# Kernel optimization log

Measured on AMD Instinct MI355X. Metric: run time of the kernel, lower is better.

The kernel has to match this reference:

```python
import jax, jax.numpy as jnp
import numpy as np

B, S, D, F, H, E = 4, 1024, 512, 2048, 8, 8
LN_EPS = 1e-5


def setup_inputs() -> dict:
    key = jax.random.key(0)
    ks = jax.random.split(key, 8)
    sd = 1.0 / np.sqrt(D)
    return {
        'x': jax.random.normal(ks[0], (B, S, D), jnp.float32),
        'in_proj_w': jax.random.normal(ks[1], (3 * D, D), jnp.float32) * sd,
        'in_proj_b': jnp.zeros((3 * D,), jnp.float32),
        'out_proj_w': jax.random.normal(ks[2], (D, D), jnp.float32) * sd,
        'out_proj_b': jnp.zeros((D,), jnp.float32),
        'ln1_g': jnp.ones((D,), jnp.float32),
        'ln1_b': jnp.zeros((D,), jnp.float32),
        'ln2_g': jnp.ones((D,), jnp.float32),
        'ln2_b': jnp.zeros((D,), jnp.float32),
        'router_w': jax.random.normal(ks[3], (D, E), jnp.float32) * sd,
        'wi': jax.random.normal(ks[4], (E, D, F), jnp.float32) * sd,
        'wo': jax.random.normal(ks[5], (E, F, D), jnp.float32) * (1.0 / np.sqrt(F)),
        'expert_capacity': 256,
    }


def _layernorm(x, g, b):
    mu = jnp.mean(x, axis=-1, keepdims=True)
    var = jnp.var(x, axis=-1, keepdims=True)
    return (x - mu) * jax.lax.rsqrt(var + LN_EPS) * g + b


def _mha(x, in_w, in_b, out_w, out_b):
    # torch nn.MultiheadAttention, batch_first, self-attention, no mask
    qkv = x @ in_w.T + in_b                         # [B,S,3D]
    q, k, v = jnp.split(qkv, 3, axis=-1)
    hd = D // H

    def heads(t):
        return t.reshape(B, S, H, hd).transpose(0, 2, 1, 3)  # [B,H,S,hd]

    q, k, v = heads(q), heads(k), heads(v)
    scores = jnp.einsum('bhqd,bhkd->bhqk', q, k) / np.sqrt(hd)
    attn = jax.nn.softmax(scores, axis=-1)
    o = jnp.einsum('bhqk,bhkd->bhqd', attn, v)
    o = o.transpose(0, 2, 1, 3).reshape(B, S, D)
    return o @ out_w.T + out_b


def _router(x, router_w, capacity):
    # Switch-style top-1 router with per-(batch,expert) capacity
    logits = x.astype(jnp.float32) @ router_w       # [B,S,E]
    probs = jax.nn.softmax(logits, axis=-1)
    idx = jnp.argmax(probs, axis=-1)                # [B,S]
    one_hot = jax.nn.one_hot(idx, E, dtype=probs.dtype)
    pos = jnp.cumsum(one_hot, axis=1)               # position within each expert queue
    keep = one_hot * (pos <= capacity).astype(probs.dtype)
    expert_mask = keep * probs                      # dispatch mask scaled by router prob
    return expert_mask, probs, logits


def reference(x, in_proj_w, in_proj_b, out_proj_w, out_proj_b,
              ln1_g, ln1_b, ln2_g, ln2_b, router_w, wi, wo, expert_capacity):
    # self-attention block (post-norm)
    residual = x
    a = _mha(x, in_proj_w, in_proj_b, out_proj_w, out_proj_b)
    h = _layernorm(residual + a, ln1_g, ln1_b)

    # sparse MoE FFN
    expert_mask, _, router_logits = _router(h, router_w, expert_capacity)
    residual = h
    moe = jnp.zeros_like(h)
    for e in range(E):  # fixed small expert loop; masked-dense == gather/FFN/scatter
        y = jax.nn.gelu(h @ wi[e], approximate=False) @ wo[e]
        moe = moe + expert_mask[..., e:e + 1] * y

    out = _layernorm(residual + moe, ln2_g, ln2_b)
    return out, router_logits, expert_mask
```

## Files before the change

### kernel.cpp

```cpp
#include <hip/hip_runtime.h>
#include <math.h>

#define SEQ 1024
#define NTOK 4096
#define DM 512
#define FF 2048
#define NE 8

typedef __attribute__((ext_vector_type(8))) short bf16x8;
typedef __attribute__((ext_vector_type(4))) float f32x4;

__device__ __forceinline__ short f2bf(float f) {
  unsigned u = __float_as_uint(f);
  unsigned r = (u + 0x7FFFu + ((u >> 16) & 1u)) >> 16;
  return (short)r;
}
__device__ __forceinline__ float bf2f(short h) {
  return __uint_as_float(((unsigned)(unsigned short)h) << 16);
}

#define GLOAD_LDS16(g, l) __builtin_amdgcn_global_load_lds( \
    (const __attribute__((address_space(1))) void*)(g),     \
    (__attribute__((address_space(3))) void*)(l), 16, 0, 0)

__global__ __launch_bounds__(256) void split3_kernel(
    const float* __restrict__ x, short* __restrict__ xh, short* __restrict__ xl,
    const float* __restrict__ w1, short* __restrict__ w1h, short* __restrict__ w1l,
    const float* __restrict__ w2, short* __restrict__ w2h, short* __restrict__ w2l) {
  const int bid = blockIdx.x;
  const float* src; short* hi; short* lo; size_t off;
  if (bid < 1024)      { src = x;  hi = xh;  lo = xl;  off = (size_t)bid * 2048; }
  else if (bid < 1408) { src = w1; hi = w1h; lo = w1l; off = (size_t)(bid - 1024) * 2048; }
  else                 { src = w2; hi = w2h; lo = w2l; off = (size_t)(bid - 1408) * 2048; }
  const size_t base = off + threadIdx.x * 8;
  float4 v0 = *reinterpret_cast<const float4*>(src + base);
  float4 v1 = *reinterpret_cast<const float4*>(src + base + 4);
  short h[8]; short l[8];
  float v[8] = {v0.x, v0.y, v0.z, v0.w, v1.x, v1.y, v1.z, v1.w};
#pragma unroll
  for (int i = 0; i < 8; ++i) {
    h[i] = f2bf(v[i]);
    l[i] = f2bf(v[i] - bf2f(h[i]));
  }
  *reinterpret_cast<short4*>(hi + base)     = make_short4(h[0], h[1], h[2], h[3]);
  *reinterpret_cast<short4*>(hi + base + 4) = make_short4(h[4], h[5], h[6], h[7]);
  *reinterpret_cast<short4*>(lo + base)     = make_short4(l[0], l[1], l[2], l[3]);
  *reinterpret_cast<short4*>(lo + base + 4) = make_short4(l[4], l[5], l[6], l[7]);
}

__global__ __launch_bounds__(256) void gemm_split_db(const short* __restrict__ Ah, const short* __restrict__ Al,
    const short* __restrict__ Bh, const short* __restrict__ Bl,
    const float* __restrict__ bias, const float* __restrict__ resid, float* __restrict__ C,
    int N, int K) {
  __shared__ __align__(16) short AsH[2][2048], AsL[2][2048], BsH[2][2048], BsL[2][2048];
  const int n0 = blockIdx.x * 64, m0 = blockIdx.y * 64;
  const int tid = threadIdx.x;
  const int lane = tid & 63, w = tid >> 6;
  const int quad = lane >> 4, l15 = lane & 15;
  const int wm = (w & 1) * 32, wn = (w >> 1) * 32;
  const int sr = tid >> 2, sc = (tid & 3) * 8;
  const short* Ahp = Ah + (size_t)(m0 + sr) * K + sc;
  const short* Alp = Al + (size_t)(m0 + sr) * K + sc;
  const short* Bhp = Bh + (size_t)(n0 + sr) * K + sc;
  const short* Blp = Bl + (size_t)(n0 + sr) * K + sc;
  GLOAD_LDS16(Ahp, &AsH[0][tid * 8]);
  GLOAD_LDS16(Alp, &AsL[0][tid * 8]);
  GLOAD_LDS16(Bhp, &BsH[0][tid * 8]);
  GLOAD_LDS16(Blp, &BsL[0][tid * 8]);
  __syncthreads();
  f32x4 acc[2][2];
#pragma unroll
  for (int i = 0; i < 2; ++i)
#pragma unroll
    for (int j = 0; j < 2; ++j) acc[i][j] = (f32x4){0.f, 0.f, 0.f, 0.f};
  for (int kt = 0; kt < K; kt += 32) {
    const int cur = (kt >> 5) & 1;
    if (kt + 32 < K) {
      const int nxt = cur ^ 1;
      GLOAD_LDS16(Ahp + kt + 32, &AsH[nxt][tid * 8]);
      GLOAD_LDS16(Alp + kt + 32, &AsL[nxt][tid * 8]);
      GLOAD_LDS16(Bhp + kt + 32, &BsH[nxt][tid * 8]);
      GLOAD_LDS16(Blp + kt + 32, &BsL[nxt][tid * 8]);
    }
    bf16x8 ah[2], al[2], bh[2], bl[2];
#pragma unroll
    for (int i = 0; i < 2; ++i) {
      ah[i] = *reinterpret_cast<const bf16x8*>(&AsH[cur][(wm + i * 16 + l15) * 32 + quad * 8]);
      al[i] = *reinterpret_cast<const bf16x8*>(&AsL[cur][(wm + i * 16 + l15) * 32 + quad * 8]);
      bh[i] = *reinterpret_cast<const bf16x8*>(&BsH[cur][(wn + i * 16 + l15) * 32 + quad * 8]);
      bl[i] = *reinterpret_cast<const bf16x8*>(&BsL[cur][(wn + i * 16 + l15) * 32 + quad * 8]);
    }
#pragma unroll
    for (int i = 0; i < 2; ++i)
#pragma unroll
      for (int j = 0; j < 2; ++j) {
        acc[i][j] = __builtin_amdgcn_mfma_f32_16x16x32_bf16(al[i], bh[j], acc[i][j], 0, 0, 0);
        acc[i][j] = __builtin_amdgcn_mfma_f32_16x16x32_bf16(ah[i], bl[j], acc[i][j], 0, 0, 0);
        acc[i][j] = __builtin_amdgcn_mfma_f32_16x16x32_bf16(ah[i], bh[j], acc[i][j], 0, 0, 0);
      }
    __syncthreads();
  }
#pragma unroll
  for (int i = 0; i < 2; ++i) {
#pragma unroll
    for (int reg = 0; reg < 4; ++reg) {
      const int row = m0 + wm + i * 16 + quad * 4 + reg;
#pragma unroll
      for (int j = 0; j < 2; ++j) {
        const int col = n0 + wn + j * 16 + l15;
        float v = acc[i][j][reg] + bias[col] + resid[(size_t)row * N + col];
        C[(size_t)row * N + col] = v;
      }
    }
  }
}

__global__ __launch_bounds__(256) void gemm_split_qkv(const short* __restrict__ Ah, const short* __restrict__ Al,
    const short* __restrict__ Bh, const short* __restrict__ Bl, const float* __restrict__ bias,
    short* __restrict__ qkh, short* __restrict__ qkl, short* __restrict__ vh, short* __restrict__ vl) {
  const int K = DM;
  __shared__ __align__(16) short AsH[2][2048], AsL[2][2048], BsH[2][2048], BsL[2][2048];
  const int n0 = blockIdx.x * 64, m0 = blockIdx.y * 64;
  const int tid = threadIdx.x;
  const int lane = tid & 63, w = tid >> 6;
  const int quad = lane >> 4, l15 = lane & 15;
  const int wm = (w & 1) * 32, wn = (w >> 1) * 32;
  const int sr = tid >> 2, sc = (tid & 3) * 8;
  const short* Ahp = Ah + (size_t)(m0 + sr) * K + sc;
  const short* Alp = Al + (size_t)(m0 + sr) * K + sc;
  const short* Bhp = Bh + (size_t)(n0 + sr) * K + sc;
  const short* Blp = Bl + (size_t)(n0 + sr) * K + sc;
  GLOAD_LDS16(Ahp, &AsH[0][tid * 8]);
  GLOAD_LDS16(Alp, &AsL[0][tid * 8]);
  GLOAD_LDS16(Bhp, &BsH[0][tid * 8]);
  GLOAD_LDS16(Blp, &BsL[0][tid * 8]);
  __syncthreads();
  f32x4 acc[2][2];
#pragma unroll
  for (int i = 0; i < 2; ++i)
#pragma unroll
    for (int j = 0; j < 2; ++j) acc[i][j] = (f32x4){0.f, 0.f, 0.f, 0.f};
  for (int kt = 0; kt < K; kt += 32) {
    const int cur = (kt >> 5) & 1;
    if (kt + 32 < K) {
      const int nxt = cur ^ 1;
      GLOAD_LDS16(Ahp + kt + 32, &AsH[nxt][tid * 8]);
      GLOAD_LDS16(Alp + kt + 32, &AsL[nxt][tid * 8]);
      GLOAD_LDS16(Bhp + kt + 32, &BsH[nxt][tid * 8]);
      GLOAD_LDS16(Blp + kt + 32, &BsL[nxt][tid * 8]);
    }
    bf16x8 ah[2], al[2], bh[2], bl[2];
#pragma unroll
    for (int i = 0; i < 2; ++i) {
      ah[i] = *reinterpret_cast<const bf16x8*>(&AsH[cur][(wm + i * 16 + l15) * 32 + quad * 8]);
      al[i] = *reinterpret_cast<const bf16x8*>(&AsL[cur][(wm + i * 16 + l15) * 32 + quad * 8]);
      bh[i] = *reinterpret_cast<const bf16x8*>(&BsH[cur][(wn + i * 16 + l15) * 32 + quad * 8]);
      bl[i] = *reinterpret_cast<const bf16x8*>(&BsL[cur][(wn + i * 16 + l15) * 32 + quad * 8]);
    }
#pragma unroll
    for (int i = 0; i < 2; ++i)
#pragma unroll
      for (int j = 0; j < 2; ++j) {
        acc[i][j] = __builtin_amdgcn_mfma_f32_16x16x32_bf16(al[i], bh[j], acc[i][j], 0, 0, 0);
        acc[i][j] = __builtin_amdgcn_mfma_f32_16x16x32_bf16(ah[i], bl[j], acc[i][j], 0, 0, 0);
        acc[i][j] = __builtin_amdgcn_mfma_f32_16x16x32_bf16(ah[i], bh[j], acc[i][j], 0, 0, 0);
      }
    __syncthreads();
  }
  if (n0 < 1024) {
#pragma unroll
    for (int i = 0; i < 2; ++i) {
#pragma unroll
      for (int reg = 0; reg < 4; ++reg) {
        const int row = m0 + wm + i * 16 + quad * 4 + reg;
#pragma unroll
        for (int j = 0; j < 2; ++j) {
          const int col = n0 + wn + j * 16 + l15;
          float v = acc[i][j][reg] + bias[col];
          short hv = f2bf(v);
          size_t ad = (size_t)row * 1024 + col;
          qkh[ad] = hv;
          qkl[ad] = f2bf(v - bf2f(hv));
        }
      }
    }
  } else {
#pragma unroll
    for (int i = 0; i < 2; ++i) {
      const int row0 = m0 + wm + i * 16 + quad * 4;
      const int bb = row0 >> 10, s0 = row0 & 1023;
#pragma unroll
      for (int j = 0; j < 2; ++j) {
        const int col = n0 + wn + j * 16 + l15;
        const int c2 = col - 1024;
        const int hhd = c2 >> 6, d = c2 & 63;
        const float bc = bias[col];
        float v0 = acc[i][j][0] + bc, v1 = acc[i][j][1] + bc, v2 = acc[i][j][2] + bc, v3 = acc[i][j][3] + bc;
        short4 hv = make_short4(f2bf(v0), f2bf(v1), f2bf(v2), f2bf(v3));
        short4 lv = make_short4(f2bf(v0 - bf2f(hv.x)), f2bf(v1 - bf2f(hv.y)),
                                f2bf(v2 - bf2f(hv.z)), f2bf(v3 - bf2f(hv.w)));
        size_t ad = ((size_t)(bb * 8 + hhd) * 64 + d) * 1024 + s0;
        *reinterpret_cast<short4*>(vh + ad) = hv;
        *reinterpret_cast<short4*>(vl + ad) = lv;
      }
    }
  }
}

__global__ __launch_bounds__(256) void attn_mfma(const short* __restrict__ qkh, const short* __restrict__ qkl,
    const short* __restrict__ vth, const short* __restrict__ vtl,
    float* __restrict__ opart, float* __restrict__ ml) {
  const int qt = blockIdx.x, hh = blockIdx.y;
  const int b = blockIdx.z >> 1, ks = blockIdx.z & 1;
  __shared__ __align__(16) short Kh[4096], Kl[4096], Vh[4096], Vl[4096];
  const int tid = threadIdx.x;
  const int lane = tid & 63, w = tid >> 6;
  const int quad = lane >> 4, l15 = lane & 15;
  const int tok0 = b * SEQ + qt * 64;
  const int srow = tid >> 2, schunk = (tid & 3) * 8;
  bf16x8 qfh[2], qfl[2];
  {
    const size_t qa = (size_t)(tok0 + w * 16 + l15) * 1024 + hh * 64 + quad * 8;
    qfh[0] = *reinterpret_cast<const bf16x8*>(qkh + qa);
    qfh[1] = *reinterpret_cast<const bf16x8*>(qkh + qa + 32);
    qfl[0] = *reinterpret_cast<const bf16x8*>(qkl + qa);
    qfl[1] = *reinterpret_cast<const bf16x8*>(qkl + qa + 32);
  }
  f32x4 oacc[4];
  float m_run[4], l_run[4];
#pragma unroll
  for (int r = 0; r < 4; ++r) { oacc[r] = (f32x4){0.f, 0.f, 0.f, 0.f}; m_run[r] = -1e30f; l_run[r] = 0.f; }
  const size_t kbase = (size_t)(b * SEQ) * 1024 + 512 + hh * 64;
  const size_t vbase = (size_t)(b * 8 + hh) * 64 * 1024;
  for (int kc = ks * 8; kc < ks * 8 + 8; ++kc) {
    const size_t ka = kbase + (size_t)(kc * 64 + srow) * 1024 + schunk;
    GLOAD_LDS16(qkh + ka,      &Kh[tid * 8]);
    GLOAD_LDS16(qkh + ka + 32, &Kh[2048 + tid * 8]);
    GLOAD_LDS16(qkl + ka,      &Kl[tid * 8]);
    GLOAD_LDS16(qkl + ka + 32, &Kl[2048 + tid * 8]);
    const size_t va = vbase + (size_t)srow * 1024 + kc * 64 + schunk;
    GLOAD_LDS16(vth + va,      &Vh[tid * 8]);
    GLOAD_LDS16(vth + va + 32, &Vh[2048 + tid * 8]);
    GLOAD_LDS16(vtl + va,      &Vl[tid * 8]);
    GLOAD_LDS16(vtl + va + 32, &Vl[2048 + tid * 8]);
    __syncthreads();
    f32x4 s[4];
#pragma unroll
    for (int j = 0; j < 4; ++j) s[j] = (f32x4){0.f, 0.f, 0.f, 0.f};
#pragma unroll
    for (int kk = 0; kk < 2; ++kk)
#pragma unroll
      for (int j = 0; j < 4; ++j) {
        bf16x8 kfh = *reinterpret_cast<const bf16x8*>(&Kh[kk * 2048 + (j * 16 + l15) * 32 + quad * 8]);
        bf16x8 kfl = *reinterpret_cast<const bf16x8*>(&Kl[kk * 2048 + (j * 16 + l15) * 32 + quad * 8]);
        s[j] = __builtin_amdgcn_mfma_f32_16x16x32_bf16(qfl[kk], kfh, s[j], 0, 0, 0);
        s[j] = __builtin_amdgcn_mfma_f32_16x16x32_bf16(qfh[kk], kfl, s[j], 0, 0, 0);
        s[j] = __builtin_amdgcn_mfma_f32_16x16x32_bf16(qfh[kk], kfh, s[j], 0, 0, 0);
      }
    __syncthreads();
    float pv[4][4], alpha[4];
#pragma unroll
    for (int reg = 0; reg < 4; ++reg) {
      float mc = fmaxf(fmaxf(s[0][reg], s[1][reg]), fmaxf(s[2][reg], s[3][reg]));
#pragma unroll
      for (int msk = 1; msk < 16; msk <<= 1) mc = fmaxf(mc, __shfl_xor(mc, msk, 64));
      mc *= 0.125f;
      float mn = fmaxf(m_run[reg], mc);
      alpha[reg] = expf(m_run[reg] - mn);
      m_run[reg] = mn;
      float pl = 0.f;
#pragma unroll
      for (int j = 0; j < 4; ++j) { float pp = expf(s[j][reg] * 0.125f - mn); pv[j][reg] = pp; pl += pp; }
#pragma unroll
      for (int msk = 1; msk < 16; msk <<= 1) pl += __shfl_xor(pl, msk, 64);
      l_run[reg] = l_run[reg] * alpha[reg] + pl;
    }
#pragma unroll
    for (int j = 0; j < 4; ++j) {
      oacc[j][0] *= alpha[0]; oacc[j][1] *= alpha[1]; oacc[j][2] *= alpha[2]; oacc[j][3] *= alpha[3];
    }
#pragma unroll
    for (int j = 0; j < 4; ++j) {
      const int cad = (j >> 1) * 2048 + (j & 1) * 16 + l15;
#pragma unroll
      for (int reg = 0; reg < 4; ++reg) {
        const int ad = cad + (w * 16 + quad * 4 + reg) * 32;
        float p = pv[j][reg];
        short hp = f2bf(p);
        Kh[ad] = hp;
        Kl[ad] = f2bf(p - bf2f(hp));
      }
    }
#pragma unroll
    for (int kk = 0; kk < 2; ++kk) {
      bf16x8 pfh = *reinterpret_cast<const bf16x8*>(&Kh[kk * 2048 + (w * 16 + l15) * 32 + quad * 8]);
      bf16x8 pfl = *reinterpret_cast<const bf16x8*>(&Kl[kk * 2048 + (w * 16 + l15) * 32 + quad * 8]);
#pragma unroll
      for (int j = 0; j < 4; ++j) {
        bf16x8 vfh = *reinterpret_cast<const bf16x8*>(&Vh[kk * 2048 + (j * 16 + l15) * 32 + quad * 8]);
        bf16x8 vfl = *reinterpret_cast<const bf16x8*>(&Vl[kk * 2048 + (j * 16 + l15) * 32 + quad * 8]);
        oacc[j] = __builtin_amdgcn_mfma_f32_16x16x32_bf16(pfl, vfh, oacc[j], 0, 0, 0);
        oacc[j] = __builtin_amdgcn_mfma_f32_16x16x32_bf16(pfh, vfl, oacc[j], 0, 0, 0);
        oacc[j] = __builtin_amdgcn_mfma_f32_16x16x32_bf16(pfh, vfh, oacc[j], 0, 0, 0);
      }
    }
    __syncthreads();
  }
  float* op = opart + (size_t)ks * 2097152;
#pragma unroll
  for (int reg = 0; reg < 4; ++reg) {
    const int rloc = w * 16 + quad * 4 + reg;
#pragma unroll
    for (int j = 0; j < 4; ++j)
      op[(size_t)(tok0 + rloc) * 512 + hh * 64 + j * 16 + l15] = oacc[j][reg];
    if (l15 == 0) {
      size_t mli = (((size_t)ks * 32 + b * 8 + hh) * 1024 + qt * 64 + rloc) * 2;
      ml[mli] = m_run[reg];
      ml[mli + 1] = l_run[reg];
    }
  }
}

__global__ __launch_bounds__(64) void combine_attn(const float* __restrict__ opart, const float* __restrict__ ml,
    short* __restrict__ oh, short* __restrict__ ol) {
  const int t = blockIdx.x;
  const int b = t >> 10, s = t & 1023;
  const int tid = threadIdx.x;
#pragma unroll
  for (int hh = 0; hh < 8; ++hh) {
    size_t mli = (((size_t)(b * 8 + hh)) * 1024 + s) * 2;
    float m0 = ml[mli], l0 = ml[mli + 1];
    float m1 = ml[65536 + mli], l1 = ml[65536 + mli + 1];
    float mm = fmaxf(m0, m1);
    float a0 = expf(m0 - mm), a1 = expf(m1 - mm);
    float inv = 1.f / (l0 * a0 + l1 * a1);
    size_t ad = (size_t)t * 512 + hh * 64 + tid;
    float v = (opart[ad] * a0 + opart[2097152 + ad] * a1) * inv;
    short hv = f2bf(v);
    oh[ad] = hv;
    ol[ad] = f2bf(v - bf2f(hv));
  }
}

__global__ __launch_bounds__(64) void ln_router(const float* __restrict__ r1,
    const float* __restrict__ g, const float* __restrict__ bta, const float* __restrict__ rw,
    float* __restrict__ h, float* __restrict__ rlog, float* __restrict__ probs, int* __restrict__ am) {
  const int t = blockIdx.x, tid = threadIdx.x;
  const size_t base = (size_t)t * DM + tid * 8;
  float4 v0 = *reinterpret_cast<const float4*>(r1 + base);
  float4 v1 = *reinterpret_cast<const float4*>(r1 + base + 4);
  float s = v0.x+v0.y+v0.z+v0.w + v1.x+v1.y+v1.z+v1.w;
  float q = v0.x*v0.x+v0.y*v0.y+v0.z*v0.z+v0.w*v0.w + v1.x*v1.x+v1.y*v1.y+v1.z*v1.z+v1.w*v1.w;
#pragma unroll
  for (int m = 1; m < 64; m <<= 1) { s += __shfl_xor(s, m, 64); q += __shfl_xor(q, m, 64); }
  float mean = s * (1.0f/512.0f);
  float var = q * (1.0f/512.0f) - mean * mean;
  float rs = rsqrtf(var + 1e-5f);
  float4 g0 = *reinterpret_cast<const float4*>(g + tid*8);
  float4 g1 = *reinterpret_cast<const float4*>(g + tid*8 + 4);
  float4 b0 = *reinterpret_cast<const float4*>(bta + tid*8);
  float4 b1 = *reinterpret_cast<const float4*>(bta + tid*8 + 4);
  float hv[8];
  hv[0] = (v0.x-mean)*rs*g0.x+b0.x; hv[1] = (v0.y-mean)*rs*g0.y+b0.y;
  hv[2] = (v0.z-mean)*rs*g0.z+b0.z; hv[3] = (v0.w-mean)*rs*g0.w+b0.w;
  hv[4] = (v1.x-mean)*rs*g1.x+b1.x; hv[5] = (v1.y-mean)*rs*g1.y+b1.y;
  hv[6] = (v1.z-mean)*rs*g1.z+b1.z; hv[7] = (v1.w-mean)*rs*g1.w+b1.w;
  *reinterpret_cast<float4*>(h + base)     = make_float4(hv[0], hv[1], hv[2], hv[3]);
  *reinterpret_cast<float4*>(h + base + 4) = make_float4(hv[4], hv[5], hv[6], hv[7]);
  float lg[8] = {0.f,0.f,0.f,0.f,0.f,0.f,0.f,0.f};
  const float* rwp = rw + tid * 64;
#pragma unroll
  for (int r = 0; r < 8; ++r) {
    float4 w0 = *reinterpret_cast<const float4*>(rwp + r * 8);
    float4 w1 = *reinterpret_cast<const float4*>(rwp + r * 8 + 4);
    float hr = hv[r];
    lg[0] += hr * w0.x; lg[1] += hr * w0.y; lg[2] += hr * w0.z; lg[3] += hr * w0.w;
    lg[4] += hr * w1.x; lg[5] += hr * w1.y; lg[6] += hr * w1.z; lg[7] += hr * w1.w;
  }
#pragma unroll
  for (int m = 1; m < 64; m <<= 1) {
#pragma unroll
    for (int e = 0; e < 8; ++e) lg[e] += __shfl_xor(lg[e], m, 64);
  }
  int best = 0; float bv = lg[0];
#pragma unroll
  for (int e = 1; e < 8; ++e) if (lg[e] > bv) { bv = lg[e]; best = e; }
  float se = 0.f;
#pragma unroll
  for (int e = 0; e < 8; ++e) se += expf(lg[e] - bv);
  float inv = 1.f / se;
  if (tid < 8) {
    rlog[t * 8 + tid] = lg[tid];
    probs[t * 8 + tid] = expf(lg[tid] - bv) * inv;
  }
  if (tid == 0) am[t] = best;
}

__global__ __launch_bounds__(64) void ln2_kernel(const float* __restrict__ x, const float* __restrict__ add,
    const int* __restrict__ pos, const int* __restrict__ capp,
    const float* __restrict__ g, const float* __restrict__ bta, float* __restrict__ y) {
  const int t = blockIdx.x, tid = threadIdx.x;
  const size_t base = (size_t)t * DM + tid * 8;
  float4 v0 = *reinterpret_cast<const float4*>(x + base);
  float4 v1 = *reinterpret_cast<const float4*>(x + base + 4);
  if (pos[t] <= *capp) {
    float4 a0 = *reinterpret_cast<const float4*>(add + base);
    float4 a1 = *reinterpret_cast<const float4*>(add + base + 4);
    v0.x += a0.x; v0.y += a0.y; v0.z += a0.z; v0.w += a0.w;
    v1.x += a1.x; v1.y += a1.y; v1.z += a1.z; v1.w += a1.w;
  }
  float s = v0.x+v0.y+v0.z+v0.w + v1.x+v1.y+v1.z+v1.w;
  float q = v0.x*v0.x+v0.y*v0.y+v0.z*v0.z+v0.w*v0.w + v1.x*v1.x+v1.y*v1.y+v1.z*v1.z+v1.w*v1.w;
#pragma unroll
  for (int m = 1; m < 64; m <<= 1) { s += __shfl_xor(s, m, 64); q += __shfl_xor(q, m, 64); }
  float mean = s * (1.0f/512.0f);
  float var = q * (1.0f/512.0f) - mean * mean;
  float rs = rsqrtf(var + 1e-5f);
  float4 g0 = *reinterpret_cast<const float4*>(g + tid*8);
  float4 g1 = *reinterpret_cast<const float4*>(g + tid*8 + 4);
  float4 b0 = *reinterpret_cast<const float4*>(bta + tid*8);
  float4 b1 = *reinterpret_cast<const float4*>(bta + tid*8 + 4);
  float4 o0 = make_float4((v0.x-mean)*rs*g0.x+b0.x, (v0.y-mean)*rs*g0.y+b0.y,
                          (v0.z-mean)*rs*g0.z+b0.z, (v0.w-mean)*rs*g0.w+b0.w);
  float4 o1 = make_float4((v1.x-mean)*rs*g1.x+b1.x, (v1.y-mean)*rs*g1.y+b1.y,
                          (v1.z-mean)*rs*g1.z+b1.z, (v1.w-mean)*rs*g1.w+b1.w);
  *reinterpret_cast<float4*>(y + base) = o0;
  *reinterpret_cast<float4*>(y + base + 4) = o1;
}

__global__ __launch_bounds__(256) void scan_kernel(const int* __restrict__ am, const float* __restrict__ probs,
    const int* __restrict__ capp, float* __restrict__ emask, int* __restrict__ pos, int* __restrict__ cnt) {
  const int bx = blockIdx.x;
  const int b = bx >> 3, e = bx & 7;
  const int tid = threadIdx.x;
  const int cap = *capp;
  __shared__ int arr[256];
  const int s_base = tid * 4;
  int f[4], incl[4];
  int c = 0;
#pragma unroll
  for (int i = 0; i < 4; ++i) {
    f[i] = (am[b * SEQ + s_base + i] == e) ? 1 : 0;
    c += f[i]; incl[i] = c;
  }
  arr[tid] = c;
  __syncthreads();
  for (int off = 1; off < 256; off <<= 1) {
    int v = (tid >= off) ? arr[tid - off] : 0;
    __syncthreads();
    arr[tid] += v;
    __syncthreads();
  }
  int excl = arr[tid] - c;
  int tot = arr[255];
#pragma unroll
  for (int i = 0; i < 4; ++i) {
    int token = b * SEQ + s_base + i;
    int p = excl + incl[i];
    bool kept = f[i] && (p <= cap);
    emask[(size_t)token * NE + e] = kept ? probs[token * NE + e] : 0.f;
    if (f[i]) pos[token] = p;
  }
  if (tid == 0) cnt[bx] = (tot < cap) ? tot : cap;
}

__global__ __launch_bounds__(256) void transpose2_bf16(const float* __restrict__ wi, short* __restrict__ wi_t,
    const float* __restrict__ wo, short* __restrict__ wo_t) {
  __shared__ float T[32][33];
  const int z = blockIdx.z;
  const float* W; short* Wt; int K, N, k0, n0;
  if (z < 8) { W = wi + (size_t)z * DM * FF;      Wt = wi_t + (size_t)z * DM * FF;
               K = DM; N = FF; k0 = blockIdx.y * 32; n0 = blockIdx.x * 32; }
  else       { W = wo + (size_t)(z - 8) * FF * DM; Wt = wo_t + (size_t)(z - 8) * FF * DM;
               K = FF; N = DM; k0 = blockIdx.x * 32; n0 = blockIdx.y * 32; }
  const int r = threadIdx.x >> 3, c4 = (threadIdx.x & 7) * 4;
  float4 v = *reinterpret_cast<const float4*>(&W[(size_t)(k0 + r) * N + n0 + c4]);
  T[r][c4+0] = v.x; T[r][c4+1] = v.y; T[r][c4+2] = v.z; T[r][c4+3] = v.w;
  __syncthreads();
  short4 o;
  o.x = f2bf(T[c4+0][r]); o.y = f2bf(T[c4+1][r]); o.z = f2bf(T[c4+2][r]); o.w = f2bf(T[c4+3][r]);
  *reinterpret_cast<short4*>(&Wt[(size_t)(n0 + r) * K + k0 + c4]) = o;
}

__global__ __launch_bounds__(128) void gather_kernel(const float* __restrict__ h, const int* __restrict__ am,
    const int* __restrict__ pos, const int* __restrict__ capp, const int* __restrict__ cnt,
    const float* __restrict__ probs, short* __restrict__ Gb, int* __restrict__ tok, float* __restrict__ mscale) {
  const int t = blockIdx.x;
  const int b = t >> 10;
  const int e = am[t];
  const int p = pos[t];
  if (p > *capp) return;
  int off = 0;
  for (int b2 = 0; b2 < b; ++b2) off += cnt[b2 * 8 + e];
  const int slot = off + p - 1;
  const int idx = e * 1024 + slot;
  if (threadIdx.x == 0) { tok[idx] = t; mscale[idx] = probs[t * NE + e]; }
  float4 v = *reinterpret_cast<const float4*>(h + (size_t)t * DM + threadIdx.x * 4);
  short4 o; o.x = f2bf(v.x); o.y = f2bf(v.y); o.z = f2bf(v.z); o.w = f2bf(v.w);
  *reinterpret_cast<short4*>(Gb + (size_t)idx * DM + threadIdx.x * 4) = o;
}

__global__ __launch_bounds__(256) void ffn1_mfma(const short* __restrict__ Gb, const short* __restrict__ wi_t,
    short* __restrict__ mid, const int* __restrict__ cnt) {
  const int e = blockIdx.z;
  const int tot = cnt[e] + cnt[8 + e] + cnt[16 + e] + cnt[24 + e];
  const int m0 = blockIdx.y * 64;
  if (m0 >= tot) return;
  const int n0 = blockIdx.x * 128;
  __shared__ __align__(16) short As[2][2048];
  __shared__ __align__(16) short Bs[2][4096];
  const int tid = threadIdx.x;
  const int lane = tid & 63, w = tid >> 6;
  const int quad = lane >> 4, l15 = lane & 15;
  const int wn = w * 32;
  const int sr = tid >> 2, sc = (tid & 3) * 8;
  const short* Ap  = Gb + ((size_t)e * 1024 + m0 + sr) * DM + sc;
  const short* Bp  = wi_t + (size_t)e * FF * DM + (size_t)(n0 + sr) * DM + sc;
  const short* Bp2 = wi_t + (size_t)e * FF * DM + (size_t)(n0 + 64 + sr) * DM + sc;
  GLOAD_LDS16(Ap,  &As[0][tid * 8]);
  GLOAD_LDS16(Bp,  &Bs[0][tid * 8]);
  GLOAD_LDS16(Bp2, &Bs[0][2048 + tid * 8]);
  __syncthreads();
  f32x4 acc[4][2];
#pragma unroll
  for (int i = 0; i < 4; ++i)
#pragma unroll
    for (int j = 0; j < 2; ++j) acc[i][j] = (f32x4){0.f, 0.f, 0.f, 0.f};
  for (int kt = 0; kt < DM; kt += 32) {
    const int cur = (kt >> 5) & 1;
    if (kt + 32 < DM) {
      const int nxt = cur ^ 1;
      GLOAD_LDS16(Ap + kt + 32,  &As[nxt][tid * 8]);
      GLOAD_LDS16(Bp + kt + 32,  &Bs[nxt][tid * 8]);
      GLOAD_LDS16(Bp2 + kt + 32, &Bs[nxt][2048 + tid * 8]);
    }
    bf16x8 a[4], b[2];
#pragma unroll
    for (int i = 0; i < 4; ++i) a[i] = *reinterpret_cast<const bf16x8*>(&As[cur][(i * 16 + l15) * 32 + quad * 8]);
#pragma unroll
    for (int j = 0; j < 2; ++j) b[j] = *reinterpret_cast<const bf16x8*>(&Bs[cur][(wn + j * 16 + l15) * 32 + quad * 8]);
#pragma unroll
    for (int i = 0; i < 4; ++i)
#pragma unroll
      for (int j = 0; j < 2; ++j)
        acc[i][j] = __builtin_amdgcn_mfma_f32_16x16x32_bf16(a[i], b[j], acc[i][j], 0, 0, 0);
    __syncthreads();
  }
#pragma unroll
  for (int i = 0; i < 4; ++i) {
#pragma unroll
    for (int reg = 0; reg < 4; ++reg) {
      const int row = m0 + i * 16 + quad * 4 + reg;
      short* outr = mid + ((size_t)e * 1024 + row) * FF;
#pragma unroll
      for (int j = 0; j < 2; ++j) {
        float v = acc[i][j][reg];
        float gl = 0.5f * v * (1.f + erff(v * 0.70710678118654752f));
        outr[n0 + wn + j * 16 + l15] = f2bf(gl);
      }
    }
  }
}

__global__ __launch_bounds__(256) void ffn2_mfma(const short* __restrict__ mid, const short* __restrict__ wo_t,
    const int* __restrict__ tok, const float* __restrict__ mscale, const int* __restrict__ cnt,
    float* __restrict__ moebuf) {
  const int e = blockIdx.z;
  const int tot = cnt[e] + cnt[8 + e] + cnt[16 + e] + cnt[24 + e];
  const int m0 = blockIdx.y * 64;
  if (m0 >= tot) return;
  const int n0 = blockIdx.x * 64;
  __shared__ __align__(16) short As[2][2048];
  __shared__ __align__(16) short Bs[2][2048];
  const int tid = threadIdx.x;
  const int lane = tid & 63, w = tid >> 6;
  const int quad = lane >> 4, l15 = lane & 15;
  const int wm = (w & 1) * 32, wn = (w >> 1) * 32;
  const int sr = tid >> 2, sc = (tid & 3) * 8;
  const short* Ap = mid + ((size_t)e * 1024 + m0 + sr) * FF + sc;
  const short* Bp = wo_t + (size_t)e * DM * FF + (size_t)(n0 + sr) * FF + sc;
  GLOAD_LDS16(Ap, &As[0][tid * 8]);
  GLOAD_LDS16(Bp, &Bs[0][tid * 8]);
  __syncthreads();
  f32x4 acc[2][2];
#pragma unroll
  for (int i = 0; i < 2; ++i)
#pragma unroll
    for (int j = 0; j < 2; ++j) acc[i][j] = (f32x4){0.f, 0.f, 0.f, 0.f};
  for (int kt = 0; kt < FF; kt += 32) {
    const int cur = (kt >> 5) & 1;
    if (kt + 32 < FF) {
      const int nxt = cur ^ 1;
      GLOAD_LDS16(Ap + kt + 32, &As[nxt][tid * 8]);
      GLOAD_LDS16(Bp + kt + 32, &Bs[nxt][tid * 8]);
    }
    bf16x8 a[2], b[2];
#pragma unroll
    for (int i = 0; i < 2; ++i) {
      a[i] = *reinterpret_cast<const bf16x8*>(&As[cur][(wm + i * 16 + l15) * 32 + quad * 8]);
      b[i] = *reinterpret_cast<const bf16x8*>(&Bs[cur][(wn + i * 16 + l15) * 32 + quad * 8]);
    }
#pragma unroll
    for (int i = 0; i < 2; ++i)
#pragma unroll
      for (int j = 0; j < 2; ++j)
        acc[i][j] = __builtin_amdgcn_mfma_f32_16x16x32_bf16(a[i], b[j], acc[i][j], 0, 0, 0);
    __syncthreads();
  }
#pragma unroll
  for (int i = 0; i < 2; ++i) {
#pragma unroll
    for (int reg = 0; reg < 4; ++reg) {
      const int slot = m0 + wm + i * 16 + quad * 4 + reg;
      if (slot < tot) {
        const int idx = e * 1024 + slot;
        const int t = tok[idx];
        const float scv = mscale[idx];
        float* outr = moebuf + (size_t)t * DM + n0 + wn;
#pragma unroll
        for (int j = 0; j < 2; ++j) outr[j * 16 + l15] = scv * acc[i][j][reg];
      }
    }
  }
}

extern "C" void kernel_launch(void* const* d_in, const int* in_sizes, int n_in,
                              void* d_out, int out_size, void* d_ws, size_t ws_size,
                              hipStream_t stream) {
  const float* x     = (const float*)d_in[0];
  const float* in_w  = (const float*)d_in[1];
  const float* in_b  = (const float*)d_in[2];
  const float* out_w = (const float*)d_in[3];
  const float* out_b = (const float*)d_in[4];
  const float* ln1g  = (const float*)d_in[5];
  const float* ln1b  = (const float*)d_in[6];
  const float* ln2g  = (const float*)d_in[7];
  const float* ln2b  = (const float*)d_in[8];
  const float* rw    = (const float*)d_in[9];
  const float* wi    = (const float*)d_in[10];
  const float* wo    = (const float*)d_in[11];
  const int*   capp  = (const int*)d_in[12];

  float* ws = (float*)d_ws;
  short* qkh  = (short*)ws;
  short* qkl  = (short*)(ws + 2097152);
  short* vth  = (short*)(ws + 4194304);
  short* vtl  = (short*)(ws + 5242880);
  short* Gb16 = (short*)ws;
  short* wi_t = (short*)(ws + 2097152);
  float* moebuf = ws + 6291456;
  float* r1     = ws + 8388608;
  float* h      = ws + 10485760;
  float* probs  = ws + 12582912;
  short* wo_t   = (short*)(ws + 12615680);
  float* opart  = ws + 16809984;
  float* mlbuf  = ws + 16809984 + 4194304;
  short* mid16  = (short*)(ws + 16809984);
  float* mscale = ws + 25198592;
  int* am    = (int*)(ws + 25206784);
  int* pos   = am + NTOK;
  int* cnt   = pos + NTOK;
  int* tok   = cnt + 32;
  short* sAh = (short*)(ws + 25231360);
  short* sAl = sAh + 2097152;
  short* sBh = sAl + 2097152;
  short* sBl = sBh + 786432;
  short* sCh = sBl + 786432;
  short* sCl = sCh + 262144;

  float* out   = (float*)d_out;
  float* rlog  = out + 2097152;
  float* emask = rlog + 32768;

  split3_kernel<<<1536, 256, 0, stream>>>(x, sAh, sAl, in_w, sBh, sBl, out_w, sCh, sCl);
  gemm_split_qkv<<<dim3(24, 64), 256, 0, stream>>>(sAh, sAl, sBh, sBl, in_b, qkh, qkl, vth, vtl);
  attn_mfma<<<dim3(16, 8, 8), 256, 0, stream>>>(qkh, qkl, vth, vtl, opart, mlbuf);
  combine_attn<<<NTOK, 64, 0, stream>>>(opart, mlbuf, sAh, sAl);
  gemm_split_db<<<dim3(8, 64), 256, 0, stream>>>(sAh, sAl, sCh, sCl, out_b, x, r1, DM, DM);
  transpose2_bf16<<<dim3(64, 16, 16), 256, 0, stream>>>(wi, wi_t, wo, wo_t);
  ln_router<<<NTOK, 64, 0, stream>>>(r1, ln1g, ln1b, rw, h, rlog, probs, am);
  scan_kernel<<<32, 256, 0, stream>>>(am, probs, capp, emask, pos, cnt);
  gather_kernel<<<NTOK, 128, 0, stream>>>(h, am, pos, capp, cnt, probs, Gb16, tok, mscale);
  ffn1_mfma<<<dim3(16, 16, 8), 256, 0, stream>>>(Gb16, wi_t, mid16, cnt);
  ffn2_mfma<<<dim3(8, 16, 8), 256, 0, stream>>>(mid16, wo_t, tok, mscale, cnt, moebuf);
  ln2_kernel<<<NTOK, 64, 0, stream>>>(h, moebuf, pos, capp, ln2g, ln2b, out);
}
```

Before: 352.1 us.

## Drop split-K attention and combine kernel, use dedicated padded P buffer

The attention kernel now processes all 16 key chunks in one block instead of splitting the keys across two blocks, and normalizes and writes the split-bf16 output directly. This removes the combine_attn launch and the fp32 partial-output round trip through global memory. A separate padded LDS buffer for P removes one barrier per iteration, the 1/sqrt(hd) scale is folded into the Q/K projection epilogue, and the low half of P is truncated rather than rounded. In exchange the grid shrinks from 1024 to 512 blocks and LDS use grows, which may lower occupancy and parallelism.

```diff
diff --git a/kernel.cpp b/kernel.cpp
--- a/kernel.cpp
+++ b/kernel.cpp
@@ -168,6 +168,7 @@
     __syncthreads();
   }
   if (n0 < 1024) {
+    const float qs = (n0 >= 512) ? 0.125f : 1.0f;
 #pragma unroll
     for (int i = 0; i < 2; ++i) {
 #pragma unroll
@@ -176,7 +177,7 @@
 #pragma unroll
         for (int j = 0; j < 2; ++j) {
           const int col = n0 + wn + j * 16 + l15;
-          float v = acc[i][j][reg] + bias[col];
+          float v = (acc[i][j][reg] + bias[col]) * qs;
           short hv = f2bf(v);
           size_t ad = (size_t)row * 1024 + col;
           qkh[ad] = hv;
@@ -207,12 +208,13 @@
   }
 }
 
+#define PSTRIDE 72
 __global__ __launch_bounds__(256) void attn_mfma(const short* __restrict__ qkh, const short* __restrict__ qkl,
     const short* __restrict__ vth, const short* __restrict__ vtl,
-    float* __restrict__ opart, float* __restrict__ ml) {
-  const int qt = blockIdx.x, hh = blockIdx.y;
-  const int b = blockIdx.z >> 1, ks = blockIdx.z & 1;
+    short* __restrict__ oh, short* __restrict__ ol) {
+  const int qt = blockIdx.x, hh = blockIdx.y, b = blockIdx.z;
   __shared__ __align__(16) short Kh[4096], Kl[4096], Vh[4096], Vl[4096];
+  __shared__ __align__(16) short Ph[64 * PSTRIDE], Pl[64 * PSTRIDE];
   const int tid = threadIdx.x;
   const int lane = tid & 63, w = tid >> 6;
   const int quad = lane >> 4, l15 = lane & 15;
@@ -232,7 +234,7 @@
   for (int r = 0; r < 4; ++r) { oacc[r] = (f32x4){0.f, 0.f, 0.f, 0.f}; m_run[r] = -1e30f; l_run[r] = 0.f; }
   const size_t kbase = (size_t)(b * SEQ) * 1024 + 512 + hh * 64;
   const size_t vbase = (size_t)(b * 8 + hh) * 64 * 1024;
-  for (int kc = ks * 8; kc < ks * 8 + 8; ++kc) {
+  for (int kc = 0; kc < 16; ++kc) {
     const size_t ka = kbase + (size_t)(kc * 64 + srow) * 1024 + schunk;
     GLOAD_LDS16(qkh + ka,      &Kh[tid * 8]);
     GLOAD_LDS16(qkh + ka + 32, &Kh[2048 + tid * 8]);
@@ -257,20 +259,18 @@
         s[j] = __builtin_amdgcn_mfma_f32_16x16x32_bf16(qfh[kk], kfl, s[j], 0, 0, 0);
         s[j] = __builtin_amdgcn_mfma_f32_16x16x32_bf16(qfh[kk], kfh, s[j], 0, 0, 0);
       }
-    __syncthreads();
     float pv[4][4], alpha[4];
 #pragma unroll
     for (int reg = 0; reg < 4; ++reg) {
       float mc = fmaxf(fmaxf(s[0][reg], s[1][reg]), fmaxf(s[2][reg], s[3][reg]));
 #pragma unroll
       for (int msk = 1; msk < 16; msk <<= 1) mc = fmaxf(mc, __shfl_xor(mc, msk, 64));
-      mc *= 0.125f;
       float mn = fmaxf(m_run[reg], mc);
       alpha[reg] = expf(m_run[reg] - mn);
       m_run[reg] = mn;
       float pl = 0.f;
 #pragma unroll
-      for (int j = 0; j < 4; ++j) { float pp = expf(s[j][reg] * 0.125f - mn); pv[j][reg] = pp; pl += pp; }
+      for (int j = 0; j < 4; ++j) { float pp = expf(s[j][reg] - mn); pv[j][reg] = pp; pl += pp; }
 #pragma unroll
       for (int msk = 1; msk < 16; msk <<= 1) pl += __shfl_xor(pl, msk, 64);
       l_run[reg] = l_run[reg] * alpha[reg] + pl;
@@ -281,20 +281,20 @@
     }
 #pragma unroll
     for (int j = 0; j < 4; ++j) {
-      const int cad = (j >> 1) * 2048 + (j & 1) * 16 + l15;
+      const int cbase = j * 16 + l15;
 #pragma unroll
       for (int reg = 0; reg < 4; ++reg) {
-        const int ad = cad + (w * 16 + quad * 4 + reg) * 32;
+        const int ad = (w * 16 + quad * 4 + reg) * PSTRIDE + cbase;
         float p = pv[j][reg];
         short hp = f2bf(p);
-        Kh[ad] = hp;
-        Kl[ad] = f2bf(p - bf2f(hp));
+        Ph[ad] = hp;
+        Pl[ad] = (short)(__float_as_uint(p - bf2f(hp)) >> 16);
       }
     }
 #pragma unroll
     for (int kk = 0; kk < 2; ++kk) {
-      bf16x8 pfh = *reinterpret_cast<const bf16x8*>(&Kh[kk * 2048 + (w * 16 + l15) * 32 + quad * 8]);
-      bf16x8 pfl = *reinterpret_cast<const bf16x8*>(&Kl[kk * 2048 + (w * 16 + l15) * 32 + quad * 8]);
+      bf16x8 pfh = *reinterpret_cast<const bf16x8*>(&Ph[(w * 16 + l15) * PSTRIDE + kk * 32 + quad * 8]);
+      bf16x8 pfl = *reinterpret_cast<const bf16x8*>(&Pl[(w * 16 + l15) * PSTRIDE + kk * 32 + quad * 8]);
 #pragma unroll
       for (int j = 0; j < 4; ++j) {
         bf16x8 vfh = *reinterpret_cast<const bf16x8*>(&Vh[kk * 2048 + (j * 16 + l15) * 32 + quad * 8]);
@@ -306,39 +306,17 @@
     }
     __syncthreads();
   }
-  float* op = opart + (size_t)ks * 2097152;
 #pragma unroll
   for (int reg = 0; reg < 4; ++reg) {
-    const int rloc = w * 16 + quad * 4 + reg;
-#pragma unroll
-    for (int j = 0; j < 4; ++j)
-      op[(size_t)(tok0 + rloc) * 512 + hh * 64 + j * 16 + l15] = oacc[j][reg];
-    if (l15 == 0) {
-      size_t mli = (((size_t)ks * 32 + b * 8 + hh) * 1024 + qt * 64 + rloc) * 2;
-      ml[mli] = m_run[reg];
-      ml[mli + 1] = l_run[reg];
-    }
-  }
-}
-
-__global__ __launch_bounds__(64) void combine_attn(const float* __restrict__ opart, const float* __restrict__ ml,
-    short* __restrict__ oh, short* __restrict__ ol) {
-  const int t = blockIdx.x;
-  const int b = t >> 10, s = t & 1023;
-  const int tid = threadIdx.x;
-#pragma unroll
-  for (int hh = 0; hh < 8; ++hh) {
-    size_t mli = (((size_t)(b * 8 + hh)) * 1024 + s) * 2;
-    float m0 = ml[mli], l0 = ml[mli + 1];
-    float m1 = ml[65536 + mli], l1 = ml[65536 + mli + 1];
-    float mm = fmaxf(m0, m1);
-    float a0 = expf(m0 - mm), a1 = expf(m1 - mm);
-    float inv = 1.f / (l0 * a0 + l1 * a1);
-    size_t ad = (size_t)t * 512 + hh * 64 + tid;
-    float v = (opart[ad] * a0 + opart[2097152 + ad] * a1) * inv;
-    short hv = f2bf(v);
-    oh[ad] = hv;
-    ol[ad] = f2bf(v - bf2f(hv));
+    const float inv = 1.f / l_run[reg];
+#pragma unroll
+    for (int j = 0; j < 4; ++j) {
+      float v = oacc[j][reg] * inv;
+      size_t ad = (size_t)(tok0 + w * 16 + quad * 4 + reg) * 512 + hh * 64 + j * 16 + l15;
+      short hv = f2bf(v);
+      oh[ad] = hv;
+      ol[ad] = f2bf(v - bf2f(hv));
+    }
   }
 }
 
@@ -653,8 +631,6 @@
   float* h      = ws + 10485760;
   float* probs  = ws + 12582912;
   short* wo_t   = (short*)(ws + 12615680);
-  float* opart  = ws + 16809984;
-  float* mlbuf  = ws + 16809984 + 4194304;
   short* mid16  = (short*)(ws + 16809984);
   float* mscale = ws + 25198592;
   int* am    = (int*)(ws + 25206784);
@@ -674,8 +650,7 @@
 
   split3_kernel<<<1536, 256, 0, stream>>>(x, sAh, sAl, in_w, sBh, sBl, out_w, sCh, sCl);
   gemm_split_qkv<<<dim3(24, 64), 256, 0, stream>>>(sAh, sAl, sBh, sBl, in_b, qkh, qkl, vth, vtl);
-  attn_mfma<<<dim3(16, 8, 8), 256, 0, stream>>>(qkh, qkl, vth, vtl, opart, mlbuf);
-  combine_attn<<<NTOK, 64, 0, stream>>>(opart, mlbuf, sAh, sAl);
+  attn_mfma<<<dim3(16, 8, 4), 256, 0, stream>>>(qkh, qkl, vth, vtl, sAh, sAl);
   gemm_split_db<<<dim3(8, 64), 256, 0, stream>>>(sAh, sAl, sCh, sCl, out_b, x, r1, DM, DM);
   transpose2_bf16<<<dim3(64, 16, 16), 256, 0, stream>>>(wi, wi_t, wo, wo_t);
   ln_router<<<NTOK, 64, 0, stream>>>(r1, ln1g, ln1b, rw, h, rlog, probs, am);
```

Measured after the change: 351.4 us. Within noise of the previous version (-0.2%).
